# Kernel tuning notes

Hardware: AMD Instinct MI355X
Metric: run time of the kernel (lower is better)

Reference implementation:

```python
import jax, jax.numpy as jnp
import numpy as np

MARGIN = 0.5


def _pairwise_dist(x):
    # Euclidean cdist via ||a||^2 + ||b||^2 - 2ab, with safe sqrt.
    sq = jnp.sum(x * x, axis=-1)  # (N,)
    d2 = sq[:, None] + sq[None, :] - 2.0 * (x @ x.T)
    d2 = jnp.maximum(d2, 0.0)
    return jnp.sqrt(jnp.where(d2 > 0.0, d2, 1.0)) * (d2 > 0.0)


def setup_inputs() -> dict:
    key = jax.random.key(0)
    k1, k2 = jax.random.split(key)
    N, D = 8192, 128
    embeddings = jax.random.normal(k1, (N, D), dtype=jnp.float32)
    labels = jax.random.randint(k2, (N,), 0, 7, dtype=jnp.int64)
    return {"embeddings": embeddings, "labels": labels}


def reference(embeddings, labels):
    N = embeddings.shape[0]
    dist = _pairwise_dist(embeddings)  # (N, N)
    same = labels[:, None] == labels[None, :]
    eye = jnp.eye(N, dtype=bool)
    pos_mask = same & ~eye
    neg_mask = ~same
    big = jnp.asarray(jnp.finfo(dist.dtype).max, dist.dtype)
    # hardest positive: max dist among same-label (excl. self)
    pos_dist = jnp.max(jnp.where(pos_mask, dist, -big), axis=1)
    # hardest negative: min dist among different-label
    neg_dist = jnp.min(jnp.where(neg_mask, dist, big), axis=1)
    valid = jnp.any(pos_mask, axis=1) & jnp.any(neg_mask, axis=1)
    per_row = jax.nn.relu(pos_dist - neg_dist + MARGIN)
    loss_sum = jnp.sum(jnp.where(valid, per_row, 0.0))
    count = jnp.sum(valid)
    return loss_sum / jnp.maximum(count, 1).astype(loss_sum.dtype)
```

## Files before the change

kernel.cpp:

```cpp
#include <hip/hip_runtime.h>

#define N 8192
#define D 128
#define MARGIN 0.5f
#define FLT_BIG 3.402823466e+38f
#define NBLK 1056

typedef __bf16 bf16x8 __attribute__((ext_vector_type(8)));
typedef float f32x4 __attribute__((ext_vector_type(4)));
typedef unsigned short u16x8 __attribute__((ext_vector_type(8)));

__device__ __forceinline__ unsigned short f2bf_rne(float f) {
  unsigned u = __float_as_uint(f);
  u += 0x7FFFu + ((u >> 16) & 1u);
  return (unsigned short)(u >> 16);
}

__device__ __forceinline__ unsigned fkey(float f) {
  unsigned u = __float_as_uint(f);
  return ((int)u < 0) ? ~u : (u | 0x80000000u);
}
__device__ __forceinline__ float fkey_inv(unsigned k) {
  unsigned u = ((int)k < 0) ? (k & 0x7FFFFFFFu) : ~k;
  return __uint_as_float(u);
}

#define FRAG_OFF(tile, k, lane) ((size_t)(tile) * 2048 + (size_t)(k) * 512 + (size_t)(lane) * 8)

__global__ void k_prep(const float* __restrict__ x, const int* __restrict__ lab,
                       unsigned short* __restrict__ xb, float* __restrict__ sq,
                       unsigned* __restrict__ posw, unsigned* __restrict__ negw,
                       unsigned* __restrict__ hist, float* __restrict__ acc,
                       unsigned* __restrict__ ticket) {
  const int t = threadIdx.x;
  const int row = blockIdx.x * 16 + (t >> 4);
  const int c = t & 15;
  const float4 v0 = ((const float4*)x)[row * 32 + c * 2];
  const float4 v1 = ((const float4*)x)[row * 32 + c * 2 + 1];
  u16x8 o;
  o[0] = f2bf_rne(v0.x); o[1] = f2bf_rne(v0.y);
  o[2] = f2bf_rne(v0.z); o[3] = f2bf_rne(v0.w);
  o[4] = f2bf_rne(v1.x); o[5] = f2bf_rne(v1.y);
  o[6] = f2bf_rne(v1.z); o[7] = f2bf_rne(v1.w);
  *(u16x8*)(xb + FRAG_OFF(row >> 4, c >> 2, ((c & 3) * 16) + (row & 15))) = o;
  float s = v0.x * v0.x + v0.y * v0.y + v0.z * v0.z + v0.w * v0.w +
            v1.x * v1.x + v1.y * v1.y + v1.z * v1.z + v1.w * v1.w;
#pragma unroll
  for (int off = 1; off < 16; off <<= 1) s += __shfl_xor(s, off, 64);
  if (c == 0) {
    sq[row] = s;
    posw[row] = 0u;
    negw[row] = 0x7F800000u;
  }

  if (blockIdx.x == 0) {
    __shared__ unsigned h[8];
    if (t < 8) h[t] = 0u;
    __syncthreads();
    unsigned long long cA = 0ull, cB = 0ull;
#pragma unroll
    for (int it = 0; it < 32; ++it) {
      const int l = lab[t + it * 256] & 7;
      if (l < 4) cA += 1ull << (l * 16);
      else       cB += 1ull << ((l - 4) * 16);
    }
#pragma unroll
    for (int off = 1; off < 64; off <<= 1) {
      cA += __shfl_xor(cA, off, 64);
      cB += __shfl_xor(cB, off, 64);
    }
    if ((t & 63) == 0) {
#pragma unroll
      for (int q = 0; q < 4; ++q) {
        atomicAdd(&h[q],     (unsigned)((cA >> (q * 16)) & 0xFFFFu));
        atomicAdd(&h[4 + q], (unsigned)((cB >> (q * 16)) & 0xFFFFu));
      }
    }
    __syncthreads();
    if (t < 8) hist[t] = h[t];
    if (t == 0) { acc[0] = 0.f; acc[1] = 0.f; ticket[0] = 0u; }
  }
}

__global__ __launch_bounds__(256)
__attribute__((amdgpu_waves_per_eu(4, 4)))
void k_mine(
    const unsigned short* __restrict__ xb, const float* __restrict__ sq,
    const int* __restrict__ lab, unsigned* __restrict__ posw, unsigned* __restrict__ negw) {
  __shared__ unsigned cposk[256], cnegk[256];

  const int t = threadIdx.x;
  const int w = t >> 6;
  const int lane = t & 63;
  const int col = lane & 15;
  const int quad = lane >> 4;

  int bj, bi;
  {
    const int T = blockIdx.x;
    int b = (int)((sqrtf((float)(4 * T + 1)) - 1.0f) * 0.5f);
    while (b * (b + 1) > T) --b;
    while ((b + 1) * (b + 2) <= T) ++b;
    bj = b;
    bi = T - b * (b + 1);
  }
  const bool diag = ((bi >> 1) == bj);
  const int i0 = bi * 128 + w * 32;
  const int jbase = bj * 256;

  cposk[t] = 0u;
  cnegk[t] = 0xFFFFFFFFu;
  __syncthreads();

  bf16x8 a[2][4];
#pragma unroll
  for (int is = 0; is < 2; ++is)
#pragma unroll
    for (int k = 0; k < 4; ++k)
      a[is][k] = *(const bf16x8*)(xb + FRAG_OFF((i0 >> 4) + is, k, lane));

  int labi[2][4];
  float sqi[2][4];
#pragma unroll
  for (int is = 0; is < 2; ++is)
#pragma unroll
    for (int r = 0; r < 4; ++r) {
      const int i = i0 + is * 16 + quad * 4 + r;
      labi[is][r] = lab[i];
      sqi[is][r] = sq[i];
    }

  float pos[2][4], neg[2][4];
#pragma unroll
  for (int is = 0; is < 2; ++is)
#pragma unroll
    for (int r = 0; r < 4; ++r) { pos[is][r] = -FLT_BIG; neg[is][r] = FLT_BIG; }

  const float* sqp = sq + jbase + col;
  const int* labp = lab + jbase + col;
  const unsigned short* gb = xb + FRAG_OFF(jbase >> 4, 0, lane);

  bf16x8 b0A, b1A, b2A, b3A, b0B, b1B, b2B, b3B;
  float sqjA, sqjB;
  int labjA, labjB;

#define LOADB(S, js_) do {                                        \
    const unsigned short* g = gb + (size_t)(js_) * 2048;          \
    b0##S = *(const bf16x8*)(g);                                  \
    b1##S = *(const bf16x8*)(g + 512);                            \
    b2##S = *(const bf16x8*)(g + 1024);                           \
    b3##S = *(const bf16x8*)(g + 1536);                           \
    sqj##S = sqp[(js_) * 16];                                     \
    labj##S = labp[(js_) * 16];                                   \
  } while (0)

#define COMPUTE(S, js_) do {                                                   \
    f32x4 acc0 = {0.f, 0.f, 0.f, 0.f}, acc1 = {0.f, 0.f, 0.f, 0.f};           \
    acc0 = __builtin_amdgcn_mfma_f32_16x16x32_bf16(a[0][0], b0##S, acc0, 0, 0, 0); \
    acc1 = __builtin_amdgcn_mfma_f32_16x16x32_bf16(a[1][0], b0##S, acc1, 0, 0, 0); \
    acc0 = __builtin_amdgcn_mfma_f32_16x16x32_bf16(a[0][1], b1##S, acc0, 0, 0, 0); \
    acc1 = __builtin_amdgcn_mfma_f32_16x16x32_bf16(a[1][1], b1##S, acc1, 0, 0, 0); \
    acc0 = __builtin_amdgcn_mfma_f32_16x16x32_bf16(a[0][2], b2##S, acc0, 0, 0, 0); \
    acc1 = __builtin_amdgcn_mfma_f32_16x16x32_bf16(a[1][2], b2##S, acc1, 0, 0, 0); \
    acc0 = __builtin_amdgcn_mfma_f32_16x16x32_bf16(a[0][3], b3##S, acc0, 0, 0, 0); \
    acc1 = __builtin_amdgcn_mfma_f32_16x16x32_bf16(a[1][3], b3##S, acc1, 0, 0, 0); \
    float cp = -FLT_BIG, cn = FLT_BIG;                                         \
    _Pragma("unroll")                                                          \
    for (int r = 0; r < 4; ++r) {                                              \
      const float m0 = fmaf(-2.f, acc0[r], sqj##S);                            \
      const float m1 = fmaf(-2.f, acc1[r], sqj##S);                            \
      const bool s0 = (labi[0][r] == labj##S);                                 \
      const bool s1 = (labi[1][r] == labj##S);                                 \
      pos[0][r] = fmaxf(pos[0][r], s0 ? m0 : -FLT_BIG);                        \
      neg[0][r] = fminf(neg[0][r], s0 ? FLT_BIG : m0);                         \
      pos[1][r] = fmaxf(pos[1][r], s1 ? m1 : -FLT_BIG);                        \
      neg[1][r] = fminf(neg[1][r], s1 ? FLT_BIG : m1);                         \
      if (!diag) {                                                             \
        const float mc0 = fmaf(-2.f, acc0[r], sqi[0][r]);                      \
        const float mc1 = fmaf(-2.f, acc1[r], sqi[1][r]);                      \
        cp = fmaxf(cp, s0 ? mc0 : -FLT_BIG);                                   \
        cn = fminf(cn, s0 ? FLT_BIG : mc0);                                    \
        cp = fmaxf(cp, s1 ? mc1 : -FLT_BIG);                                   \
        cn = fminf(cn, s1 ? FLT_BIG : mc1);                                    \
      }                                                                        \
    }                                                                          \
    if (!diag) {                                                               \
      cp = fmaxf(cp, __shfl_xor(cp, 16, 64));                                  \
      cp = fmaxf(cp, __shfl_xor(cp, 32, 64));                                  \
      cn = fminf(cn, __shfl_xor(cn, 16, 64));                                  \
      cn = fminf(cn, __shfl_xor(cn, 32, 64));                                  \
      if (quad == 0) {                                                         \
        atomicMax(&cposk[(js_) * 16 + col], fkey(cp));                         \
        atomicMin(&cnegk[(js_) * 16 + col], fkey(cn));                         \
      }                                                                        \
    }                                                                          \
  } while (0)

  LOADB(A, 0);
#pragma unroll 1
  for (int js = 0; js < 14; js += 2) {
    LOADB(B, js + 1);
    COMPUTE(A, js);
    LOADB(A, js + 2);
    COMPUTE(B, js + 1);
  }
  LOADB(B, 15);
  COMPUTE(A, 14);
  COMPUTE(B, 15);

#undef LOADB
#undef COMPUTE

#pragma unroll
  for (int is = 0; is < 2; ++is)
#pragma unroll
    for (int r = 0; r < 4; ++r) {
      float p = pos[is][r], n = neg[is][r];
#pragma unroll
      for (int off = 1; off < 16; off <<= 1) {
        p = fmaxf(p, __shfl_xor(p, off, 64));
        n = fminf(n, __shfl_xor(n, off, 64));
      }
      if (col == 0) {
        const int i = i0 + is * 16 + quad * 4 + r;
        atomicMax(posw + i, __float_as_uint(fmaxf(sqi[is][r] + p, 0.f)));
        atomicMin(negw + i, __float_as_uint(fmaxf(sqi[is][r] + n, 0.f)));
      }
    }

  if (!diag) {
    __syncthreads();
    const int j = jbase + t;
    const float cpv = fkey_inv(cposk[t]);
    const float cnv = fkey_inv(cnegk[t]);
    const float sqj = sq[j];
    atomicMax(posw + j, __float_as_uint(fmaxf(sqj + cpv, 0.f)));
    atomicMin(negw + j, __float_as_uint(fmaxf(sqj + cnv, 0.f)));
  }
}

__global__ void k_tail(const unsigned* __restrict__ posw, const unsigned* __restrict__ negw,
                       const int* __restrict__ lab, const unsigned* __restrict__ hist,
                       float* __restrict__ acc, unsigned* __restrict__ ticket,
                       float* __restrict__ out) {
  __shared__ float ls[4], cs[4];
  const int t = threadIdx.x;
  const int i = blockIdx.x * 256 + t;
  const float pd2 = __uint_as_float(posw[i]);
  const float nd2 = __uint_as_float(negw[i]);
  const unsigned cnt = hist[lab[i] & 7];
  const bool valid = (cnt >= 2u) && (cnt < (unsigned)N);
  float loss = 0.f, c = 0.f;
  if (valid) {
    loss = fmaxf(sqrtf(pd2) - sqrtf(fminf(nd2, FLT_BIG)) + MARGIN, 0.f);
    c = 1.f;
  }
#pragma unroll
  for (int off = 1; off < 64; off <<= 1) {
    loss += __shfl_xor(loss, off, 64);
    c += __shfl_xor(c, off, 64);
  }
  const int wv = t >> 6;
  if ((t & 63) == 0) { ls[wv] = loss; cs[wv] = c; }
  __syncthreads();
  if (t == 0) {
    atomicAdd(acc + 0, ls[0] + ls[1] + ls[2] + ls[3]);
    atomicAdd(acc + 1, cs[0] + cs[1] + cs[2] + cs[3]);
    __threadfence();
    const unsigned tk = atomicAdd(ticket, 1u);
    if (tk == 31u) {
      const float lsum = atomicAdd(acc + 0, 0.f);
      const float csum = atomicAdd(acc + 1, 0.f);
      out[0] = lsum / fmaxf(csum, 1.f);
    }
  }
}

extern "C" void kernel_launch(void* const* d_in, const int* in_sizes, int n_in,
                              void* d_out, int out_size, void* d_ws, size_t ws_size,
                              hipStream_t stream) {
  const float* x = (const float*)d_in[0];
  const int* lab = (const int*)d_in[1];
  char* ws = (char*)d_ws;
  unsigned short* xb = (unsigned short*)ws;
  float* sq = (float*)(ws + (size_t)N * D * 2);
  unsigned* posw = (unsigned*)((char*)sq + (size_t)N * 4);
  unsigned* negw = posw + N;
  unsigned* hist = negw + N;
  unsigned* ticket = hist + 8;
  float* acc = (float*)(ticket + 1);
  float* out = (float*)d_out;

  hipLaunchKernelGGL(k_prep, dim3(512), dim3(256), 0, stream, x, lab, xb, sq,
                     posw, negw, hist, acc, ticket);
  hipLaunchKernelGGL(k_mine, dim3(NBLK), dim3(256), 0, stream, xb, sq, lab, posw, negw);
  hipLaunchKernelGGL(k_tail, dim3(32), dim3(256), 0, stream, posw, negw, lab, hist,
                     acc, ticket, out);
}
```

Before: 97.81 us.

## Exploit symmetry within diagonal blocks by computing only upper-triangular tiles

Diagonal 256-wide column blocks no longer compute the full 256x256 square without the transposed update. Each wave now does two triangular passes that cover only the upper triangle of 32x16 sub-tiles and also apply the column-side update. Off-diagonal blocks map to full 128x256 tiles with the column update. This cuts the grid from 1056 to 1024 blocks and removes redundant MFMA work on diagonal blocks, at the cost of a per-wave pass loop and some duplicated work on the diagonal sub-tiles.

```diff
diff --git a/kernel.cpp b/kernel.cpp
--- a/kernel.cpp
+++ b/kernel.cpp
@@ -4,7 +4,7 @@
 #define D 128
 #define MARGIN 0.5f
 #define FLT_BIG 3.402823466e+38f
-#define NBLK 1056
+#define NBLK 1024
 
 typedef __bf16 bf16x8 __attribute__((ext_vector_type(8)));
 typedef float f32x4 __attribute__((ext_vector_type(4)));
@@ -95,54 +95,35 @@
   const int col = lane & 15;
   const int quad = lane >> 4;
 
-  int bj, bi;
+  int bj, tile0, js0, tile1, js1, npass;
   {
     const int T = blockIdx.x;
-    int b = (int)((sqrtf((float)(4 * T + 1)) - 1.0f) * 0.5f);
-    while (b * (b + 1) > T) --b;
-    while ((b + 1) * (b + 2) <= T) ++b;
-    bj = b;
-    bi = T - b * (b + 1);
-  }
-  const bool diag = ((bi >> 1) == bj);
-  const int i0 = bi * 128 + w * 32;
+    if (T < 32) {
+      bj = T;
+      npass = 2;
+      tile0 = bj * 16 + 2 * w;        js0 = 2 * w;
+      tile1 = bj * 16 + 14 - 2 * w;   js1 = 14 - 2 * w;
+    } else {
+      const int Tp = T - 32;
+      int b = (int)((1.0f + sqrtf((float)(4 * Tp + 1))) * 0.5f);
+      while (b * (b - 1) > Tp) --b;
+      while (b * (b + 1) <= Tp) ++b;
+      bj = b;
+      const int bi = Tp - b * (b - 1);
+      npass = 1;
+      tile0 = bi * 8 + 2 * w;  js0 = 0;
+      tile1 = 0;               js1 = 0;
+    }
+  }
   const int jbase = bj * 256;
 
   cposk[t] = 0u;
   cnegk[t] = 0xFFFFFFFFu;
   __syncthreads();
 
-  bf16x8 a[2][4];
-#pragma unroll
-  for (int is = 0; is < 2; ++is)
-#pragma unroll
-    for (int k = 0; k < 4; ++k)
-      a[is][k] = *(const bf16x8*)(xb + FRAG_OFF((i0 >> 4) + is, k, lane));
-
-  int labi[2][4];
-  float sqi[2][4];
-#pragma unroll
-  for (int is = 0; is < 2; ++is)
-#pragma unroll
-    for (int r = 0; r < 4; ++r) {
-      const int i = i0 + is * 16 + quad * 4 + r;
-      labi[is][r] = lab[i];
-      sqi[is][r] = sq[i];
-    }
-
-  float pos[2][4], neg[2][4];
-#pragma unroll
-  for (int is = 0; is < 2; ++is)
-#pragma unroll
-    for (int r = 0; r < 4; ++r) { pos[is][r] = -FLT_BIG; neg[is][r] = FLT_BIG; }
-
   const float* sqp = sq + jbase + col;
   const int* labp = lab + jbase + col;
   const unsigned short* gb = xb + FRAG_OFF(jbase >> 4, 0, lane);
-
-  bf16x8 b0A, b1A, b2A, b3A, b0B, b1B, b2B, b3B;
-  float sqjA, sqjB;
-  int labjA, labjB;
 
 #define LOADB(S, js_) do {                                        \
     const unsigned short* g = gb + (size_t)(js_) * 2048;          \
@@ -175,61 +156,91 @@
       neg[0][r] = fminf(neg[0][r], s0 ? FLT_BIG : m0);                         \
       pos[1][r] = fmaxf(pos[1][r], s1 ? m1 : -FLT_BIG);                        \
       neg[1][r] = fminf(neg[1][r], s1 ? FLT_BIG : m1);                         \
-      if (!diag) {                                                             \
-        const float mc0 = fmaf(-2.f, acc0[r], sqi[0][r]);                      \
-        const float mc1 = fmaf(-2.f, acc1[r], sqi[1][r]);                      \
-        cp = fmaxf(cp, s0 ? mc0 : -FLT_BIG);                                   \
-        cn = fminf(cn, s0 ? FLT_BIG : mc0);                                    \
-        cp = fmaxf(cp, s1 ? mc1 : -FLT_BIG);                                   \
-        cn = fminf(cn, s1 ? FLT_BIG : mc1);                                    \
-      }                                                                        \
+      const float mc0 = fmaf(-2.f, acc0[r], sqi[0][r]);                        \
+      const float mc1 = fmaf(-2.f, acc1[r], sqi[1][r]);                        \
+      cp = fmaxf(cp, s0 ? mc0 : -FLT_BIG);                                     \
+      cn = fminf(cn, s0 ? FLT_BIG : mc0);                                      \
+      cp = fmaxf(cp, s1 ? mc1 : -FLT_BIG);                                     \
+      cn = fminf(cn, s1 ? FLT_BIG : mc1);                                      \
     }                                                                          \
-    if (!diag) {                                                               \
-      cp = fmaxf(cp, __shfl_xor(cp, 16, 64));                                  \
-      cp = fmaxf(cp, __shfl_xor(cp, 32, 64));                                  \
-      cn = fminf(cn, __shfl_xor(cn, 16, 64));                                  \
-      cn = fminf(cn, __shfl_xor(cn, 32, 64));                                  \
-      if (quad == 0) {                                                         \
-        atomicMax(&cposk[(js_) * 16 + col], fkey(cp));                         \
-        atomicMin(&cnegk[(js_) * 16 + col], fkey(cn));                         \
-      }                                                                        \
+    cp = fmaxf(cp, __shfl_xor(cp, 16, 64));                                    \
+    cp = fmaxf(cp, __shfl_xor(cp, 32, 64));                                    \
+    cn = fminf(cn, __shfl_xor(cn, 16, 64));                                    \
+    cn = fminf(cn, __shfl_xor(cn, 32, 64));                                    \
+    if (quad == 0) {                                                           \
+      atomicMax(&cposk[(js_) * 16 + col], fkey(cp));                           \
+      atomicMin(&cnegk[(js_) * 16 + col], fkey(cn));                           \
     }                                                                          \
   } while (0)
 
-  LOADB(A, 0);
 #pragma unroll 1
-  for (int js = 0; js < 14; js += 2) {
-    LOADB(B, js + 1);
-    COMPUTE(A, js);
-    LOADB(A, js + 2);
-    COMPUTE(B, js + 1);
-  }
-  LOADB(B, 15);
-  COMPUTE(A, 14);
-  COMPUTE(B, 15);
+  for (int p = 0; p < npass; ++p) {
+    const int tA = (p == 0) ? tile0 : tile1;
+    const int s = (p == 0) ? js0 : js1;
+
+    bf16x8 a[2][4];
+#pragma unroll
+    for (int is = 0; is < 2; ++is)
+#pragma unroll
+      for (int k = 0; k < 4; ++k)
+        a[is][k] = *(const bf16x8*)(xb + FRAG_OFF(tA + is, k, lane));
+
+    int labi[2][4];
+    float sqi[2][4];
+#pragma unroll
+    for (int is = 0; is < 2; ++is)
+#pragma unroll
+      for (int r = 0; r < 4; ++r) {
+        const int i = (tA + is) * 16 + quad * 4 + r;
+        labi[is][r] = lab[i];
+        sqi[is][r] = sq[i];
+      }
+
+    float pos[2][4], neg[2][4];
+#pragma unroll
+    for (int is = 0; is < 2; ++is)
+#pragma unroll
+      for (int r = 0; r < 4; ++r) { pos[is][r] = -FLT_BIG; neg[is][r] = FLT_BIG; }
+
+    bf16x8 b0A, b1A, b2A, b3A, b0B, b1B, b2B, b3B;
+    float sqjA, sqjB;
+    int labjA, labjB;
+
+    LOADB(A, s);
+#pragma unroll 1
+    for (int js = s; js < 14; js += 2) {
+      LOADB(B, js + 1);
+      COMPUTE(A, js);
+      LOADB(A, js + 2);
+      COMPUTE(B, js + 1);
+    }
+    LOADB(B, 15);
+    COMPUTE(A, 14);
+    COMPUTE(B, 15);
+
+#pragma unroll
+    for (int is = 0; is < 2; ++is)
+#pragma unroll
+      for (int r = 0; r < 4; ++r) {
+        float p2 = pos[is][r], n2 = neg[is][r];
+#pragma unroll
+        for (int off = 1; off < 16; off <<= 1) {
+          p2 = fmaxf(p2, __shfl_xor(p2, off, 64));
+          n2 = fminf(n2, __shfl_xor(n2, off, 64));
+        }
+        if (col == 0) {
+          const int i = (tA + is) * 16 + quad * 4 + r;
+          atomicMax(posw + i, __float_as_uint(fmaxf(sqi[is][r] + p2, 0.f)));
+          atomicMin(negw + i, __float_as_uint(fmaxf(sqi[is][r] + n2, 0.f)));
+        }
+      }
+  }
 
 #undef LOADB
 #undef COMPUTE
 
-#pragma unroll
-  for (int is = 0; is < 2; ++is)
-#pragma unroll
-    for (int r = 0; r < 4; ++r) {
-      float p = pos[is][r], n = neg[is][r];
-#pragma unroll
-      for (int off = 1; off < 16; off <<= 1) {
-        p = fmaxf(p, __shfl_xor(p, off, 64));
-        n = fminf(n, __shfl_xor(n, off, 64));
-      }
-      if (col == 0) {
-        const int i = i0 + is * 16 + quad * 4 + r;
-        atomicMax(posw + i, __float_as_uint(fmaxf(sqi[is][r] + p, 0.f)));
-        atomicMin(negw + i, __float_as_uint(fmaxf(sqi[is][r] + n, 0.f)));
-      }
-    }
-
-  if (!diag) {
-    __syncthreads();
+  __syncthreads();
+  {
     const int j = jbase + t;
     const float cpv = fkey_inv(cposk[t]);
     const float cnv = fkey_inv(cnegk[t]);
```

After: 109.8 us. 12.3% more time.
